# Kernel optimization log

Measured on AMD Instinct MI355X. Metric: run time of the kernel, lower is better.

## Reference

```python
import jax, jax.numpy as jnp
import numpy as np

D_MODEL = 1024
NUM_HEADS = 16
HEAD_DIM = D_MODEL // NUM_HEADS
MAX_SEQ_LEN = 2048
THETA = 10000.0
B, T = 2, 2048


def precompute_cos_sin(head_dim, max_len, theta):
    freqs = 1.0 / theta ** (jnp.arange(0, head_dim, 2, dtype=jnp.float32) / head_dim)
    t = jnp.arange(max_len, dtype=jnp.float32)
    f = jnp.outer(t, freqs)  # [max_len, head_dim//2]
    return jnp.concatenate([jnp.cos(f), jnp.sin(f)], axis=-1)  # [max_len, head_dim]


def apply_rotary_emb(x, cos_sin):
    # x: [B, H, T, Hs]; cos_sin: [T, Hs]
    xr = x.reshape(*x.shape[:-1], -1, 2)
    x1, x2 = xr[..., 0], xr[..., 1]
    cos, sin = jnp.split(cos_sin, 2, axis=-1)  # each [T, Hs//2]
    out = jnp.stack([x1 * cos - x2 * sin, x1 * sin + x2 * cos], axis=-1)
    return out.reshape(x.shape).astype(x.dtype)


def setup_inputs() -> dict:
    key = jax.random.key(0)
    ks = jax.random.split(key, 5)
    scale = 1.0 / np.sqrt(D_MODEL)
    return {
        'x': jax.random.normal(ks[0], (B, T, D_MODEL), dtype=jnp.float32),
        'wq': jax.random.normal(ks[1], (D_MODEL, D_MODEL), dtype=jnp.float32) * scale,
        'wk': jax.random.normal(ks[2], (D_MODEL, D_MODEL), dtype=jnp.float32) * scale,
        'wv': jax.random.normal(ks[3], (D_MODEL, D_MODEL), dtype=jnp.float32) * scale,
        'wo': jax.random.normal(ks[4], (D_MODEL, D_MODEL), dtype=jnp.float32) * scale,
    }


def reference(x, wq, wk, wv, wo):
    seq_len = x.shape[1]
    # Linear: einsum('...i,oi->...o'), weight stored as [out, in]
    q = jnp.einsum('bti,oi->bto', x, wq)
    k = jnp.einsum('bti,oi->bto', x, wk)
    v = jnp.einsum('bti,oi->bto', x, wv)
    # split heads: B T (nH Hs) -> B nH T Hs
    def split_heads(t):
        return t.reshape(t.shape[0], t.shape[1], NUM_HEADS, HEAD_DIM).transpose(0, 2, 1, 3)
    xq, xk, xv = split_heads(q), split_heads(k), split_heads(v)
    cos_sin = precompute_cos_sin(HEAD_DIM, MAX_SEQ_LEN, THETA)[:seq_len]
    xq = apply_rotary_emb(xq, cos_sin)
    xk = apply_rotary_emb(xk, cos_sin)
    scores = jnp.einsum('bhqd,bhkd->bhqk', xq, xk) / jnp.sqrt(jnp.float32(HEAD_DIM))
    causal = jnp.tril(jnp.ones((seq_len, seq_len), dtype=bool))
    scores = jnp.where(causal[None, None], scores, -jnp.inf)
    attn = jax.nn.softmax(scores, axis=-1)
    xo = jnp.einsum('bhqk,bhkd->bhqd', attn, xv)
    xo = xo.transpose(0, 2, 1, 3).reshape(x.shape[0], seq_len, D_MODEL)
    return jnp.einsum('bti,oi->bto', xo, wo)
```

## Files before the change

kernel.cpp:

```cpp
#include <hip/hip_runtime.h>
#include <hip/hip_bf16.h>

typedef __hip_bfloat16 bf16;
using s8v = __attribute__((ext_vector_type(8))) short;
using s4v = __attribute__((ext_vector_type(4))) short;
using f4v = __attribute__((ext_vector_type(4))) float;
using f16v = __attribute__((ext_vector_type(16))) float;

#define D_MODEL 1024
#define NHEADS  16
#define HDIM    64
#define TSEQ    2048
#define NBATCH  2
#define BT      (NBATCH * TSEQ)

#define QSCALE  0.180336880111f
#define SBIAS  -17.3123404907f

__device__ inline short f2bf_bits(float f) {
    bf16 h = __float2bfloat16(f);
    return *reinterpret_cast<short*>(&h);
}

__device__ inline unsigned cvt_pk_bf16(float lo, float hi) {
    unsigned r;
    asm("v_cvt_pk_bf16_f32 %0, %1, %2" : "=v"(r) : "v"(lo), "v"(hi));
    return r;
}

__device__ inline void perm_swap(unsigned &a, unsigned &b) {
    asm volatile("v_permlane32_swap_b32 %0, %1" : "+v"(a), "+v"(b));
}

__device__ inline void load8(const bf16* p, s8v& o) { o = *(const s8v*)p; }
__device__ inline void load8(const float* p, s8v& o) {
    const f4v a = *(const f4v*)p;
    const f4v b = *(const f4v*)(p + 4);
    s8v r;
    r[0] = f2bf_bits(a[0]); r[1] = f2bf_bits(a[1]);
    r[2] = f2bf_bits(a[2]); r[3] = f2bf_bits(a[3]);
    r[4] = f2bf_bits(b[0]); r[5] = f2bf_bits(b[1]);
    r[6] = f2bf_bits(b[2]); r[7] = f2bf_bits(b[3]);
    o = r;
}

__device__ inline void storeC(bf16* p, float v)  { *p = __float2bfloat16(v); }
__device__ inline void storeC(float* p, float v) { *p = v; }

__device__ inline void gload_lds16(const bf16* g, short* l) {
    __builtin_amdgcn_global_load_lds(
        (__attribute__((address_space(1))) void*)(unsigned long long)(size_t)g,
        (__attribute__((address_space(3))) void*)l,
        16, 0, 0);
}

__device__ inline void stage8(const bf16* g, short* l) { gload_lds16(g, l); }
__device__ inline void stage8(const float* g, short* l) {
    s8v v; load8(g, v); *(s8v*)l = v;
}

__global__ __launch_bounds__(256) void cvt_kernel(
    const float* __restrict__ src, bf16* __restrict__ dst)
{
    const size_t i = ((size_t)blockIdx.x * 256 + threadIdx.x) * 8;
    s8v v; load8(src + i, v);
    *(s8v*)&dst[i] = v;
}

__global__ __launch_bounds__(256) void cvt_all_kernel(
    const float* __restrict__ x,  bf16* __restrict__ xb,
    const float* __restrict__ wq, bf16* __restrict__ wqb,
    const float* __restrict__ wk, bf16* __restrict__ wkb,
    const float* __restrict__ wv, bf16* __restrict__ wvb,
    const float* __restrict__ wo, bf16* __restrict__ wob,
    float2* __restrict__ cs_table)
{
    const int blk = blockIdx.x;
    if (blk >= 4096) {
        const int idx = (blk - 4096) * 256 + threadIdx.x;
        const int tt = idx >> 5;
        const int i  = idx & 31;
        const float inv_freq = expf(-(float)i * (9.210340371976184f / 32.0f));
        float s, c;
        sincosf((float)tt * inv_freq, &s, &c);
        cs_table[idx] = make_float2(c, s);
        return;
    }
    const float* src; bf16* dst; int base;
    if (blk < 2048)      { src = x;  dst = xb;  base = 0; }
    else if (blk < 2560) { src = wq; dst = wqb; base = 2048; }
    else if (blk < 3072) { src = wk; dst = wkb; base = 2560; }
    else if (blk < 3584) { src = wv; dst = wvb; base = 3072; }
    else                 { src = wo; dst = wob; base = 3584; }
    const size_t i = ((size_t)(blk - base) * 256 + threadIdx.x) * 8;
    s8v v; load8(src + i, v);
    *(s8v*)&dst[i] = v;
}

template <int TM, bool ROPE, typename TA, typename TW, typename TC>
__global__ __launch_bounds__(256, 2) void gemm_bt(
    const TA* __restrict__ A,
    const TW* __restrict__ W0, const TW* __restrict__ W1, const TW* __restrict__ W2,
    TC* __restrict__ C0, TC* __restrict__ C1, TC* __restrict__ C2,
    bf16* __restrict__ VT, const float2* __restrict__ cs_table)
{
    const TW* W = (blockIdx.z == 0) ? W0 : (blockIdx.z == 1) ? W1 : W2;
    TC*       C = (blockIdx.z == 0) ? C0 : (blockIdx.z == 1) ? C1 : C2;
    const bool vt_mode = (VT != nullptr) && (blockIdx.z == 2);

    constexpr int K = 1024, N = 1024;
    constexpr int MT = TM / 32;
    __shared__ __align__(16) short As[TM * 64];
    __shared__ __align__(16) short Ws[128 * 64];

    const int t    = threadIdx.x;
    const int lane = t & 63;
    const int wave = t >> 6;
    const int m16  = lane & 15;
    const int quad = lane >> 4;
    const int wm   = (wave >> 1) * (TM / 2);
    const int wn   = (wave & 1) * 64;
    const int rowBase = blockIdx.x * TM;
    const int colBase = blockIdx.y * 128;

    f4v acc[MT][4];
#pragma unroll
    for (int i = 0; i < MT; ++i)
#pragma unroll
        for (int j = 0; j < 4; ++j) acc[i][j] = f4v{0.f, 0.f, 0.f, 0.f};

    for (int kk = 0; kk < K / 64; ++kk) {
#pragma unroll
        for (int r = 0; r < TM / 32; ++r) {
            const int chunk = r * 256 + t;
            const int row   = chunk >> 3;
            const int c8s   = (chunk & 7) ^ (row & 7);
            stage8(A + (size_t)(rowBase + row) * K + kk * 64 + c8s * 8, &As[chunk * 8]);
        }
#pragma unroll
        for (int r = 0; r < 4; ++r) {
            const int chunk = r * 256 + t;
            const int row   = chunk >> 3;
            const int c8s   = (chunk & 7) ^ (row & 7);
            stage8(W + (size_t)(colBase + row) * K + kk * 64 + c8s * 8, &Ws[chunk * 8]);
        }
        __syncthreads();

#pragma unroll
        for (int ks = 0; ks < 2; ++ks) {
            s8v af[MT], bw[4];
#pragma unroll
            for (int mt = 0; mt < MT; ++mt) {
                const int rowa = wm + mt * 16 + m16;
                af[mt] = *(const s8v*)&As[rowa * 64 + ((ks * 4 + quad) ^ (rowa & 7)) * 8];
            }
#pragma unroll
            for (int nt = 0; nt < 4; ++nt) {
                const int roww = wn + nt * 16 + m16;
                bw[nt] = *(const s8v*)&Ws[roww * 64 + ((ks * 4 + quad) ^ (roww & 7)) * 8];
            }
#pragma unroll
            for (int mt = 0; mt < MT; ++mt)
#pragma unroll
                for (int nt = 0; nt < 4; ++nt)
                    acc[mt][nt] = __builtin_amdgcn_mfma_f32_16x16x32_bf16(
                        af[mt], bw[nt], acc[mt][nt], 0, 0, 0);
        }
        __syncthreads();
    }

    if (vt_mode) {
#pragma unroll
        for (int mt = 0; mt < MT; ++mt)
#pragma unroll
            for (int nt = 0; nt < 4; ++nt) {
                const int col  = colBase + wn + nt * 16 + m16;
                const int row0 = rowBase + wm + mt * 16 + quad * 4;
                const int bb   = row0 >> 11;
                const int tt   = row0 & (TSEQ - 1);
                s4v pk;
#pragma unroll
                for (int r = 0; r < 4; ++r) pk[r] = f2bf_bits(acc[mt][nt][r]);
                *(s4v*)&VT[((size_t)(bb * 1024 + col)) * TSEQ + tt] = pk;
            }
    } else {
        const float qs = (ROPE && blockIdx.z == 0) ? QSCALE : 1.0f;
#pragma unroll
        for (int mt = 0; mt < MT; ++mt)
#pragma unroll
            for (int nt = 0; nt < 4; ++nt) {
                const int col = colBase + wn + nt * 16 + m16;
#pragma unroll
                for (int r = 0; r < 4; ++r) {
                    const int row = rowBase + wm + mt * 16 + quad * 4 + r;
                    float v = acc[mt][nt][r];
                    if (ROPE) {
                        const float prt = __shfl_xor(v, 1, 64);
                        const int   tt  = row & (TSEQ - 1);
                        const int   i   = (col & 63) >> 1;
                        const float2 cs = cs_table[tt * 32 + i];
                        v = (col & 1) ? (prt * cs.y + v * cs.x)
                                      : (v * cs.x - prt * cs.y);
                        v *= qs;
                    }
                    storeC(&C[(size_t)row * N + col], v);
                }
            }
    }
}

__global__ __launch_bounds__(256) void rope_inplace(
    bf16* __restrict__ qp, bf16* __restrict__ kp)
{
    const int idx = blockIdx.x * 256 + threadIdx.x;
    const int i  = idx & 31;
    const int h  = (idx >> 5) & (NHEADS - 1);
    const int tt = (idx >> 9) & (TSEQ - 1);
    const int b  = idx >> 20;

    const size_t src = (size_t)(b * TSEQ + tt) * D_MODEL + h * HDIM + 2 * i;

    const float inv_freq = expf(-(float)i * (9.210340371976184f / 32.0f));
    const float f = (float)tt * inv_freq;
    float s, c;
    sincosf(f, &s, &c);

    const float q1 = __bfloat162float(qp[src]);
    const float q2 = __bfloat162float(qp[src + 1]);
    qp[src]     = __float2bfloat16((q1 * c - q2 * s) * QSCALE);
    qp[src + 1] = __float2bfloat16((q1 * s + q2 * c) * QSCALE);

    const float k1 = __bfloat162float(kp[src]);
    const float k2 = __bfloat162float(kp[src + 1]);
    kp[src]     = __float2bfloat16(k1 * c - k2 * s);
    kp[src + 1] = __float2bfloat16(k1 * s + k2 * c);
}

__global__ __launch_bounds__(256, 2) void attn_kernel(
    bf16* __restrict__ qp, const bf16* __restrict__ kp,
    const bf16* __restrict__ vt)
{
    const int hb = blockIdx.x & 31;
    const int ib = blockIdx.x >> 5;
    const int h  = hb & (NHEADS - 1);
    const int b  = hb >> 4;
    const int t    = threadIdx.x;
    const int lane = t & 63;
    const int wave = t >> 6;
    const int l31  = lane & 31;
    const int hi   = lane >> 5;
    const int wq   = wave >> 1;
    const int wk   = wave & 1;

    bf16*       Qb  = qp + (size_t)b * TSEQ * D_MODEL + h * HDIM;
    const bf16* Kb  = kp + (size_t)b * TSEQ * D_MODEL + h * HDIM;
    const bf16* Vtb = vt + ((size_t)b * 1024 + h * HDIM) * TSEQ;

    __shared__ __align__(16) short Klds[2][128 * 64];
    __shared__ __align__(16) short Vlds[2][64 * 128];

    auto stage_kv = [&](int buf, int kv0) {
#pragma unroll
        for (int r = 0; r < 4; ++r) {
            const int chunk = r * 256 + t;
            const int row   = chunk >> 3;
            const int c8s   = (chunk & 7) ^ (row & 7);
            gload_lds16(Kb + (size_t)(kv0 + row) * D_MODEL + c8s * 8,
                        &Klds[buf][chunk * 8]);
        }
#pragma unroll
        for (int r = 0; r < 4; ++r) {
            const int chunk = r * 256 + t;
            const int row   = chunk >> 4;
            const int c16s  = (chunk & 15) ^ (row & 15);
            gload_lds16(Vtb + (size_t)row * TSEQ + kv0 + c16s * 8,
                        &Vlds[buf][chunk * 8]);
        }
    };

#pragma unroll 1
    for (int pass = 0; pass < 2; ++pass) {
        const int bx = pass ? (31 - ib) : ib;
        const int q0 = bx * 64;
        const int qrow = q0 + wq * 32 + l31;

        const bf16* qptr = Qb + (size_t)qrow * D_MODEL;
        s8v qf[4];
#pragma unroll
        for (int s2 = 0; s2 < 4; ++s2)
            qf[s2] = *(const s8v*)&qptr[s2 * 16 + hi * 8];

        f16v o_acc[2];
#pragma unroll
        for (int db = 0; db < 2; ++db)
#pragma unroll
            for (int r = 0; r < 16; ++r) o_acc[db][r] = 0.0f;
        float l_acc = 0.0f;

        const int iters = (bx + 2) >> 1;

        stage_kv(0, 0);

#pragma unroll 1
        for (int it = 0; it < iters; ++it) {
            const int cur = it & 1;
            const int kv0 = it * 128;

            if (it + 1 < iters) {
                stage_kv(cur ^ 1, kv0 + 128);
                asm volatile("s_waitcnt vmcnt(8)" ::: "memory");
            } else {
                asm volatile("s_waitcnt vmcnt(0)" ::: "memory");
            }
            __builtin_amdgcn_s_barrier();
            __builtin_amdgcn_sched_barrier(0);

            f16v sacc[2];
            __builtin_amdgcn_s_setprio(1);
#pragma unroll
            for (int kb = 0; kb < 2; ++kb) {
                const int rowk = wk * 64 + kb * 32 + l31;
                const short* kbase = &Klds[cur][rowk * 64];
                const int r7 = rowk & 7;
                f16v acc;
#pragma unroll
                for (int r = 0; r < 16; ++r) acc[r] = SBIAS;
#pragma unroll
                for (int s2 = 0; s2 < 4; ++s2) {
                    const s8v ak = *(const s8v*)&kbase[((s2 * 2 + hi) ^ r7) * 8];
                    acc = __builtin_amdgcn_mfma_f32_32x32x16_bf16(
                        ak, qf[s2], acc, 0, 0, 0);
                }
                sacc[kb] = acc;
            }
            __builtin_amdgcn_s_setprio(0);

            const bool diag = (it == iters - 1);
#pragma unroll
            for (int kb = 0; kb < 2; ++kb) {
#pragma unroll
                for (int r = 0; r < 16; ++r) {
                    float p = __builtin_amdgcn_exp2f(sacc[kb][r]);
                    if (diag) {
                        const int kg = kv0 + wk * 64 + kb * 32
                                     + (r & 3) + 8 * (r >> 2) + 4 * hi;
                        p = (kg <= qrow) ? p : 0.0f;
                    }
                    sacc[kb][r] = p;
                    l_acc += p;
                }
            }

            __builtin_amdgcn_s_setprio(1);
#pragma unroll
            for (int s = 0; s < 4; ++s) {
                const int kb = s >> 1;
                const int h8 = (s & 1) * 8;
                unsigned w0 = cvt_pk_bf16(sacc[kb][h8 + 0], sacc[kb][h8 + 1]);
                unsigned w1 = cvt_pk_bf16(sacc[kb][h8 + 2], sacc[kb][h8 + 3]);
                unsigned w2 = cvt_pk_bf16(sacc[kb][h8 + 4], sacc[kb][h8 + 5]);
                unsigned w3 = cvt_pk_bf16(sacc[kb][h8 + 6], sacc[kb][h8 + 7]);
                perm_swap(w0, w2);
                perm_swap(w1, w3);
                union { unsigned u[4]; s8v v; } pu;
                pu.u[0] = w0; pu.u[1] = w1; pu.u[2] = w2; pu.u[3] = w3;
                const int gch = wk * 8 + s * 2 + hi;
#pragma unroll
                for (int db = 0; db < 2; ++db) {
                    const int rowd = db * 32 + l31;
                    const s8v bv = *(const s8v*)&Vlds[cur][rowd * 128
                                                    + (gch ^ (rowd & 15)) * 8];
                    o_acc[db] = __builtin_amdgcn_mfma_f32_32x32x16_bf16(
                        pu.v, bv, o_acc[db], 0, 0, 0);
                }
            }
            __builtin_amdgcn_s_setprio(0);

            asm volatile("s_waitcnt lgkmcnt(0)" ::: "memory");
            __builtin_amdgcn_s_barrier();
        }

        const float lw = l_acc + __shfl_xor(l_acc, 32, 64);
        float* Xf = (float*)&Klds[0][0];
        float* Lf = (float*)&Vlds[0][0];
        __syncthreads();

        {
            const f16v* opw = (wk == 0) ? &o_acc[1] : &o_acc[0];
#pragma unroll
            for (int r = 0; r < 16; ++r) {
                const int qo = (r & 3) + 8 * (r >> 2) + 4 * hi;
                Xf[((wq * 2 + wk) * 32 + qo) * 32 + l31] = (*opw)[r];
            }
        }
        if (lane < 32) Lf[(wq * 2 + wk) * 32 + l31] = lw;
        __syncthreads();

        {
            const f16v* opm = (wk == 0) ? &o_acc[0] : &o_acc[1];
#pragma unroll
            for (int rg = 0; rg < 4; ++rg) {
                const f4v lp0 = *(const f4v*)&Lf[(wq * 2 + 0) * 32 + rg * 8 + hi * 4];
                const f4v lp1 = *(const f4v*)&Lf[(wq * 2 + 1) * 32 + rg * 8 + hi * 4];
#pragma unroll
                for (int j = 0; j < 4; ++j) {
                    const int r  = rg * 4 + j;
                    const int qo = rg * 8 + hi * 4 + j;
                    const float oo = (*opm)[r]
                        + Xf[((wq * 2 + (1 - wk)) * 32 + qo) * 32 + l31];
                    Qb[(size_t)(q0 + wq * 32 + qo) * D_MODEL + wk * 32 + l31] =
                        __float2bfloat16(oo / (lp0[j] + lp1[j]));
                }
            }
        }
        __syncthreads();
    }
}

extern "C" void kernel_launch(void* const* d_in, const int* in_sizes, int n_in,
                              void* d_out, int out_size, void* d_ws, size_t ws_size,
                              hipStream_t stream) {
    const float* x  = (const float*)d_in[0];
    const float* wq = (const float*)d_in[1];
    const float* wk = (const float*)d_in[2];
    const float* wv = (const float*)d_in[3];
    const float* wo = (const float*)d_in[4];
    float* out = (float*)d_out;

    bf16* ws = (bf16*)d_ws;
    const size_t SZ  = (size_t)BT * D_MODEL;
    const size_t SZW = (size_t)D_MODEL * D_MODEL;
    bf16* qp  = ws + 0 * SZ;
    bf16* kp  = ws + 1 * SZ;
    bf16* vt  = (bf16*)d_out;
    bf16* xb  = (bf16*)(out + 2 * 1024 * 1024);

    const size_t need_w    = (2 * SZ + 4 * SZW) * sizeof(bf16);
    const size_t need_full = need_w + 65536 * sizeof(float2);

    if (ws_size >= need_full) {
        bf16*   wqb = ws + 2 * SZ + 0 * SZW;
        bf16*   wkb = ws + 2 * SZ + 1 * SZW;
        bf16*   wvb = ws + 2 * SZ + 2 * SZW;
        bf16*   wob = ws + 2 * SZ + 3 * SZW;
        float2* cst = (float2*)(ws + 2 * SZ + 4 * SZW);

        cvt_all_kernel<<<dim3(4352), 256, 0, stream>>>(
            x, xb, wq, wqb, wk, wkb, wv, wvb, wo, wob, cst);
        gemm_bt<128, true, bf16, bf16, bf16><<<dim3(32, 8, 3), 256, 0, stream>>>(
            xb, wqb, wkb, wvb, qp, kp, qp , vt, cst);
        attn_kernel<<<dim3(512), 256, 0, stream>>>(qp, kp, vt);
        gemm_bt<64, false, bf16, bf16, float><<<dim3(64, 8, 1), 256, 0, stream>>>(
            qp, wob, wob, wob, out, out, out, nullptr, nullptr);
    } else if (ws_size >= need_w) {
        bf16* wqb = ws + 2 * SZ + 0 * SZW;
        bf16* wkb = ws + 2 * SZ + 1 * SZW;
        bf16* wvb = ws + 2 * SZ + 2 * SZW;
        bf16* wob = ws + 2 * SZ + 3 * SZW;
        cvt_all_kernel<<<dim3(4096), 256, 0, stream>>>(
            x, xb, wq, wqb, wk, wkb, wv, wvb, wo, wob, nullptr);
        gemm_bt<128, false, bf16, bf16, bf16><<<dim3(32, 8, 3), 256, 0, stream>>>(
            xb, wqb, wkb, wvb, qp, kp, qp , vt, nullptr);
        rope_inplace<<<dim3(8192), 256, 0, stream>>>(qp, kp);
        attn_kernel<<<dim3(512), 256, 0, stream>>>(qp, kp, vt);
        gemm_bt<64, false, bf16, bf16, float><<<dim3(64, 8, 1), 256, 0, stream>>>(
            qp, wob, wob, wob, out, out, out, nullptr, nullptr);
    } else {
        bf16* wob = kp;
        cvt_kernel<<<dim3(2048), 256, 0, stream>>>(x, xb);
        gemm_bt<128, false, bf16, float, bf16><<<dim3(32, 8, 3), 256, 0, stream>>>(
            xb, wq, wk, wv, qp, kp, qp , vt, nullptr);
        rope_inplace<<<dim3(8192), 256, 0, stream>>>(qp, kp);
        attn_kernel<<<dim3(512), 256, 0, stream>>>(qp, kp, vt);
        cvt_kernel<<<dim3(512), 256, 0, stream>>>(wo, wob);
        gemm_bt<64, false, bf16, bf16, float><<<dim3(64, 8, 1), 256, 0, stream>>>(
            qp, wob, wob, wob, out, out, out, nullptr, nullptr);
    }
}
```

Before: 169.8 us.

## Enlarge attention query tile to 128 rows with 512-thread blocks

The attention kernel now has 8 waves per block, each block owning one 128-row query tile. This replaces two passes over paired 64-row tiles. Each K/V stage in LDS is therefore shared by twice as many query rows, which roughly halves K/V load traffic per query. Blocks are numbered so the longest causal tiles are scheduled first, and the score accumulator is processed one 32-column slice at a time to cut register pressure for the higher occupancy target. In exchange, the ib/31-ib pairing that balanced work across blocks is gone, so work per block is less even, and launch_bounds(512,4) may squeeze registers.

```diff
diff --git a/kernel.cpp b/kernel.cpp
--- a/kernel.cpp
+++ b/kernel.cpp
@@ -236,12 +236,12 @@
     kp[src + 1] = __float2bfloat16(k1 * s + k2 * c);
 }
 
-__global__ __launch_bounds__(256, 2) void attn_kernel(
+__global__ __launch_bounds__(512, 4) void attn_kernel(
     bf16* __restrict__ qp, const bf16* __restrict__ kp,
     const bf16* __restrict__ vt)
 {
     const int hb = blockIdx.x & 31;
-    const int ib = blockIdx.x >> 5;
+    const int bx = 15 - (blockIdx.x >> 5);
     const int h  = hb & (NHEADS - 1);
     const int b  = hb >> 4;
     const int t    = threadIdx.x;
@@ -261,16 +261,16 @@
 
     auto stage_kv = [&](int buf, int kv0) {
 #pragma unroll
-        for (int r = 0; r < 4; ++r) {
-            const int chunk = r * 256 + t;
+        for (int r = 0; r < 2; ++r) {
+            const int chunk = r * 512 + t;
             const int row   = chunk >> 3;
             const int c8s   = (chunk & 7) ^ (row & 7);
             gload_lds16(Kb + (size_t)(kv0 + row) * D_MODEL + c8s * 8,
                         &Klds[buf][chunk * 8]);
         }
 #pragma unroll
-        for (int r = 0; r < 4; ++r) {
-            const int chunk = r * 256 + t;
+        for (int r = 0; r < 2; ++r) {
+            const int chunk = r * 512 + t;
             const int row   = chunk >> 4;
             const int c16s  = (chunk & 15) ^ (row & 15);
             gload_lds16(Vtb + (size_t)row * TSEQ + kv0 + c16s * 8,
@@ -278,93 +278,84 @@
         }
     };
 
+    const int q0   = bx * 128;
+    const int qrow = q0 + wq * 32 + l31;
+
+    const bf16* qptr = Qb + (size_t)qrow * D_MODEL;
+    s8v qf[4];
+#pragma unroll
+    for (int s2 = 0; s2 < 4; ++s2)
+        qf[s2] = *(const s8v*)&qptr[s2 * 16 + hi * 8];
+
+    f16v o_acc[2];
+#pragma unroll
+    for (int db = 0; db < 2; ++db)
+#pragma unroll
+        for (int r = 0; r < 16; ++r) o_acc[db][r] = 0.0f;
+    float l_acc = 0.0f;
+
+    const int iters = bx + 1;
+
+    stage_kv(0, 0);
+
 #pragma unroll 1
-    for (int pass = 0; pass < 2; ++pass) {
-        const int bx = pass ? (31 - ib) : ib;
-        const int q0 = bx * 64;
-        const int qrow = q0 + wq * 32 + l31;
-
-        const bf16* qptr = Qb + (size_t)qrow * D_MODEL;
-        s8v qf[4];
-#pragma unroll
-        for (int s2 = 0; s2 < 4; ++s2)
-            qf[s2] = *(const s8v*)&qptr[s2 * 16 + hi * 8];
-
-        f16v o_acc[2];
-#pragma unroll
-        for (int db = 0; db < 2; ++db)
-#pragma unroll
-            for (int r = 0; r < 16; ++r) o_acc[db][r] = 0.0f;
-        float l_acc = 0.0f;
-
-        const int iters = (bx + 2) >> 1;
-
-        stage_kv(0, 0);
-
-#pragma unroll 1
-        for (int it = 0; it < iters; ++it) {
-            const int cur = it & 1;
-            const int kv0 = it * 128;
-
-            if (it + 1 < iters) {
-                stage_kv(cur ^ 1, kv0 + 128);
-                asm volatile("s_waitcnt vmcnt(8)" ::: "memory");
-            } else {
-                asm volatile("s_waitcnt vmcnt(0)" ::: "memory");
-            }
-            __builtin_amdgcn_s_barrier();
-            __builtin_amdgcn_sched_barrier(0);
-
-            f16v sacc[2];
+    for (int it = 0; it < iters; ++it) {
+        const int cur = it & 1;
+        const int kv0 = it * 128;
+
+        if (it + 1 < iters) {
+            stage_kv(cur ^ 1, kv0 + 128);
+            asm volatile("s_waitcnt vmcnt(4)" ::: "memory");
+        } else {
+            asm volatile("s_waitcnt vmcnt(0)" ::: "memory");
+        }
+        __builtin_amdgcn_s_barrier();
+        __builtin_amdgcn_sched_barrier(0);
+
+        const bool diag = (it == iters - 1);
+
+#pragma unroll
+        for (int kb = 0; kb < 2; ++kb) {
+            const int rowk = wk * 64 + kb * 32 + l31;
+            const short* kbase = &Klds[cur][rowk * 64];
+            const int r7 = rowk & 7;
+            f16v sacc;
+#pragma unroll
+            for (int r = 0; r < 16; ++r) sacc[r] = SBIAS;
             __builtin_amdgcn_s_setprio(1);
 #pragma unroll
-            for (int kb = 0; kb < 2; ++kb) {
-                const int rowk = wk * 64 + kb * 32 + l31;
-                const short* kbase = &Klds[cur][rowk * 64];
-                const int r7 = rowk & 7;
-                f16v acc;
-#pragma unroll
-                for (int r = 0; r < 16; ++r) acc[r] = SBIAS;
-#pragma unroll
-                for (int s2 = 0; s2 < 4; ++s2) {
-                    const s8v ak = *(const s8v*)&kbase[((s2 * 2 + hi) ^ r7) * 8];
-                    acc = __builtin_amdgcn_mfma_f32_32x32x16_bf16(
-                        ak, qf[s2], acc, 0, 0, 0);
+            for (int s2 = 0; s2 < 4; ++s2) {
+                const s8v ak = *(const s8v*)&kbase[((s2 * 2 + hi) ^ r7) * 8];
+                sacc = __builtin_amdgcn_mfma_f32_32x32x16_bf16(
+                    ak, qf[s2], sacc, 0, 0, 0);
+            }
+            __builtin_amdgcn_s_setprio(0);
+
+#pragma unroll
+            for (int r = 0; r < 16; ++r) {
+                float p = __builtin_amdgcn_exp2f(sacc[r]);
+                if (diag) {
+                    const int kg = kv0 + wk * 64 + kb * 32
+                                 + (r & 3) + 8 * (r >> 2) + 4 * hi;
+                    p = (kg <= qrow) ? p : 0.0f;
                 }
-                sacc[kb] = acc;
-            }
-            __builtin_amdgcn_s_setprio(0);
-
-            const bool diag = (it == iters - 1);
-#pragma unroll
-            for (int kb = 0; kb < 2; ++kb) {
-#pragma unroll
-                for (int r = 0; r < 16; ++r) {
-                    float p = __builtin_amdgcn_exp2f(sacc[kb][r]);
-                    if (diag) {
-                        const int kg = kv0 + wk * 64 + kb * 32
-                                     + (r & 3) + 8 * (r >> 2) + 4 * hi;
-                        p = (kg <= qrow) ? p : 0.0f;
-                    }
-                    sacc[kb][r] = p;
-                    l_acc += p;
-                }
+                sacc[r] = p;
+                l_acc += p;
             }
 
             __builtin_amdgcn_s_setprio(1);
 #pragma unroll
-            for (int s = 0; s < 4; ++s) {
-                const int kb = s >> 1;
-                const int h8 = (s & 1) * 8;
-                unsigned w0 = cvt_pk_bf16(sacc[kb][h8 + 0], sacc[kb][h8 + 1]);
-                unsigned w1 = cvt_pk_bf16(sacc[kb][h8 + 2], sacc[kb][h8 + 3]);
-                unsigned w2 = cvt_pk_bf16(sacc[kb][h8 + 4], sacc[kb][h8 + 5]);
-                unsigned w3 = cvt_pk_bf16(sacc[kb][h8 + 6], sacc[kb][h8 + 7]);
+            for (int sh = 0; sh < 2; ++sh) {
+                const int h8 = sh * 8;
+                unsigned w0 = cvt_pk_bf16(sacc[h8 + 0], sacc[h8 + 1]);
+                unsigned w1 = cvt_pk_bf16(sacc[h8 + 2], sacc[h8 + 3]);
+                unsigned w2 = cvt_pk_bf16(sacc[h8 + 4], sacc[h8 + 5]);
+                unsigned w3 = cvt_pk_bf16(sacc[h8 + 6], sacc[h8 + 7]);
                 perm_swap(w0, w2);
                 perm_swap(w1, w3);
                 union { unsigned u[4]; s8v v; } pu;
                 pu.u[0] = w0; pu.u[1] = w1; pu.u[2] = w2; pu.u[3] = w3;
-                const int gch = wk * 8 + s * 2 + hi;
+                const int gch = wk * 8 + (kb * 2 + sh) * 2 + hi;
 #pragma unroll
                 for (int db = 0; db < 2; ++db) {
                     const int rowd = db * 32 + l31;
@@ -375,45 +366,44 @@
                 }
             }
             __builtin_amdgcn_s_setprio(0);
-
-            asm volatile("s_waitcnt lgkmcnt(0)" ::: "memory");
-            __builtin_amdgcn_s_barrier();
-        }
-
-        const float lw = l_acc + __shfl_xor(l_acc, 32, 64);
-        float* Xf = (float*)&Klds[0][0];
-        float* Lf = (float*)&Vlds[0][0];
-        __syncthreads();
-
-        {
-            const f16v* opw = (wk == 0) ? &o_acc[1] : &o_acc[0];
-#pragma unroll
-            for (int r = 0; r < 16; ++r) {
-                const int qo = (r & 3) + 8 * (r >> 2) + 4 * hi;
-                Xf[((wq * 2 + wk) * 32 + qo) * 32 + l31] = (*opw)[r];
-            }
-        }
-        if (lane < 32) Lf[(wq * 2 + wk) * 32 + l31] = lw;
-        __syncthreads();
-
-        {
-            const f16v* opm = (wk == 0) ? &o_acc[0] : &o_acc[1];
-#pragma unroll
-            for (int rg = 0; rg < 4; ++rg) {
-                const f4v lp0 = *(const f4v*)&Lf[(wq * 2 + 0) * 32 + rg * 8 + hi * 4];
-                const f4v lp1 = *(const f4v*)&Lf[(wq * 2 + 1) * 32 + rg * 8 + hi * 4];
-#pragma unroll
-                for (int j = 0; j < 4; ++j) {
-                    const int r  = rg * 4 + j;
-                    const int qo = rg * 8 + hi * 4 + j;
-                    const float oo = (*opm)[r]
-                        + Xf[((wq * 2 + (1 - wk)) * 32 + qo) * 32 + l31];
-                    Qb[(size_t)(q0 + wq * 32 + qo) * D_MODEL + wk * 32 + l31] =
-                        __float2bfloat16(oo / (lp0[j] + lp1[j]));
-                }
-            }
-        }
-        __syncthreads();
+        }
+
+        asm volatile("s_waitcnt lgkmcnt(0)" ::: "memory");
+        __builtin_amdgcn_s_barrier();
+    }
+
+    const float lw = l_acc + __shfl_xor(l_acc, 32, 64);
+    float* Xf = (float*)&Klds[0][0];
+    float* Lf = (float*)&Vlds[0][0];
+    __syncthreads();
+
+    {
+        const f16v* opw = (wk == 0) ? &o_acc[1] : &o_acc[0];
+#pragma unroll
+        for (int r = 0; r < 16; ++r) {
+            const int qo = (r & 3) + 8 * (r >> 2) + 4 * hi;
+            Xf[((wq * 2 + wk) * 32 + qo) * 32 + l31] = (*opw)[r];
+        }
+    }
+    if (lane < 32) Lf[(wq * 2 + wk) * 32 + l31] = lw;
+    __syncthreads();
+
+    {
+        const f16v* opm = (wk == 0) ? &o_acc[0] : &o_acc[1];
+#pragma unroll
+        for (int rg = 0; rg < 4; ++rg) {
+            const f4v lp0 = *(const f4v*)&Lf[(wq * 2 + 0) * 32 + rg * 8 + hi * 4];
+            const f4v lp1 = *(const f4v*)&Lf[(wq * 2 + 1) * 32 + rg * 8 + hi * 4];
+#pragma unroll
+            for (int j = 0; j < 4; ++j) {
+                const int r  = rg * 4 + j;
+                const int qo = rg * 8 + hi * 4 + j;
+                const float oo = (*opm)[r]
+                    + Xf[((wq * 2 + (1 - wk)) * 32 + qo) * 32 + l31];
+                Qb[(size_t)(q0 + wq * 32 + qo) * D_MODEL + wk * 32 + l31] =
+                    __float2bfloat16(oo / (lp0[j] + lp1[j]));
+            }
+        }
     }
 }
 
@@ -449,7 +439,7 @@
             x, xb, wq, wqb, wk, wkb, wv, wvb, wo, wob, cst);
         gemm_bt<128, true, bf16, bf16, bf16><<<dim3(32, 8, 3), 256, 0, stream>>>(
             xb, wqb, wkb, wvb, qp, kp, qp , vt, cst);
-        attn_kernel<<<dim3(512), 256, 0, stream>>>(qp, kp, vt);
+        attn_kernel<<<dim3(512), 512, 0, stream>>>(qp, kp, vt);
         gemm_bt<64, false, bf16, bf16, float><<<dim3(64, 8, 1), 256, 0, stream>>>(
             qp, wob, wob, wob, out, out, out, nullptr, nullptr);
     } else if (ws_size >= need_w) {
@@ -462,7 +452,7 @@
         gemm_bt<128, false, bf16, bf16, bf16><<<dim3(32, 8, 3), 256, 0, stream>>>(
             xb, wqb, wkb, wvb, qp, kp, qp , vt, nullptr);
         rope_inplace<<<dim3(8192), 256, 0, stream>>>(qp, kp);
-        attn_kernel<<<dim3(512), 256, 0, stream>>>(qp, kp, vt);
+        attn_kernel<<<dim3(512), 512, 0, stream>>>(qp, kp, vt);
         gemm_bt<64, false, bf16, bf16, float><<<dim3(64, 8, 1), 256, 0, stream>>>(
             qp, wob, wob, wob, out, out, out, nullptr, nullptr);
     } else {
@@ -471,7 +461,7 @@
         gemm_bt<128, false, bf16, float, bf16><<<dim3(32, 8, 3), 256, 0, stream>>>(
             xb, wq, wk, wv, qp, kp, qp , vt, nullptr);
         rope_inplace<<<dim3(8192), 256, 0, stream>>>(qp, kp);
-        attn_kernel<<<dim3(512), 256, 0, stream>>>(qp, kp, vt);
+        attn_kernel<<<dim3(512), 512, 0, stream>>>(qp, kp, vt);
         cvt_kernel<<<dim3(512), 256, 0, stream>>>(wo, wob);
         gemm_bt<64, false, bf16, bf16, float><<<dim3(64, 8, 1), 256, 0, stream>>>(
             qp, wob, wob, wob, out, out, out, nullptr, nullptr);
```

Result: no change. 170.4 us (+0.3%).
